# Performance work log

Hardware: AMD Instinct MI355X
Metric: run time of the kernel (lower is better)

Reference implementation:

```python
import jax, jax.numpy as jnp
import numpy as np

B_, C_, NH_, WS_, HID_ = 8, 512, 16, 7, 2048
HH, WW = 56, 56


def _rel_pos_index(ws):
    coords = np.stack(np.meshgrid(np.arange(ws), np.arange(ws), indexing='ij'))  # (2,ws,ws)
    cf = coords.reshape(2, -1)
    rc = (cf[:, :, None] - cf[:, None, :]).transpose(1, 2, 0)  # (ws2,ws2,2)
    rc[..., 0] += ws - 1
    rc[..., 1] += ws - 1
    rc[..., 0] *= 2 * ws - 1
    return jnp.asarray(rc.sum(-1).reshape(-1))  # (ws2*ws2,)


def _ln(x, g, b, eps):
    mu = x.mean(-1, keepdims=True)
    var = ((x - mu) ** 2).mean(-1, keepdims=True)
    return (x - mu) * jax.lax.rsqrt(var + eps) * g + b


def setup_inputs() -> dict:
    key = jax.random.key(0)
    ks = jax.random.split(key, 8)
    s = lambda k, shape: (jax.random.normal(k, shape, jnp.float32) * 0.02)
    return {
        'x': jax.random.normal(ks[0], (B_, HH * WW, C_), jnp.float32),
        'H': HH, 'W': WW,
        'norm1_g': jnp.ones((C_,), jnp.float32), 'norm1_b': jnp.zeros((C_,), jnp.float32),
        'norm2_g': jnp.ones((C_,), jnp.float32), 'norm2_b': jnp.zeros((C_,), jnp.float32),
        'qkv_w': s(ks[1], (3 * C_, C_)), 'qkv_b': jnp.zeros((3 * C_,), jnp.float32),
        'rpb': s(ks[2], ((2 * WS_ - 1) ** 2, NH_)),
        'fc1_w': s(ks[3], (HID_, C_)), 'fc1_b': jnp.zeros((HID_,), jnp.float32),
        'dw_w': s(ks[4], (HID_, 1, 3, 3)), 'dw_b': jnp.zeros((HID_,), jnp.float32),
        'fc2_w': s(ks[5], (C_, HID_)), 'fc2_b': jnp.zeros((C_,), jnp.float32),
    }


def reference(x, H, W, norm1_g, norm1_b, norm2_g, norm2_b, qkv_w, qkv_b, rpb,
              fc1_w, fc1_b, dw_w, dw_b, fc2_w, fc2_b):
    B, N, C = x.shape
    ws, nh = WS_, NH_
    hd = C // nh
    scale = hd ** -0.5
    ws2 = ws * ws
    nHw, nWw = H // ws, W // ws

    # ---- norm1 + WaveAttention (windowed attention w/ relative position bias) ----
    h = _ln(x, norm1_g, norm1_b, 1e-5)
    qkv = h @ qkv_w.T + qkv_b                                   # [B,N,3C]
    # window partition: [B, nH, ws, nW, ws, 3, nh, hd] -> [3, B*nH*nW, nh, ws2, hd]
    qkv = qkv.reshape(B, nHw, ws, nWw, ws, 3, nh, hd)
    qkv = qkv.transpose(5, 0, 1, 3, 6, 2, 4, 7).reshape(3, B * nHw * nWw, nh, ws2, hd)
    q, k, v = qkv[0], qkv[1], qkv[2]

    attn = jnp.einsum('wnid,wnjd->wnij', q, k) * scale          # [Bw,nh,ws2,ws2]
    bias = rpb[_rel_pos_index(ws)].reshape(ws2, ws2, nh).transpose(2, 0, 1)
    attn = jax.nn.softmax(attn + bias[None], axis=-1)
    out = jnp.einsum('wnij,wnjd->wnid', attn, v)                # [Bw,nh,ws2,hd]
    # window reverse
    out = out.transpose(0, 2, 1, 3).reshape(B, nHw, nWw, ws, ws, C)
    out = out.transpose(0, 1, 3, 2, 4, 5).reshape(B, N, C)
    x = x + out

    # ---- norm2 + PVT2FFN (fc1 -> depthwise 3x3 conv -> GELU -> fc2) ----
    h2 = _ln(x, norm2_g, norm2_b, 1e-5)
    h2 = h2 @ fc1_w.T + fc1_b                                   # [B,N,HID]
    img = h2.reshape(B, H, W, HID_).transpose(0, 3, 1, 2)       # [B,HID,H,W]
    img = jax.lax.conv_general_dilated(img, dw_w, (1, 1), 'SAME',
                                       feature_group_count=HID_)
    img = img + dw_b[None, :, None, None]
    h2 = img.reshape(B, HID_, N).transpose(0, 2, 1)
    h2 = jax.nn.gelu(h2, approximate=False)
    h2 = h2 @ fc2_w.T + fc2_b
    return x + h2
```

## Files before the change

kernel.cpp:

```cpp
#include <hip/hip_runtime.h>
#include <hip/hip_bf16.h>

typedef unsigned short u16;
typedef unsigned int u32;
typedef __attribute__((ext_vector_type(8))) short bf16x8_t;
typedef __attribute__((ext_vector_type(4))) float f32x4_t;
typedef __attribute__((ext_vector_type(8))) u16 u16x8;
typedef __attribute__((ext_vector_type(4))) u32 u32x4;

constexpr int B_  = 8;
constexpr int C_  = 512;
constexpr int NH_ = 16;
constexpr int HID_= 2048;
constexpr int Hh  = 56, Ww = 56;
constexpr int N_  = Hh * Ww;
constexpr int M_  = B_ * N_;

__device__ __forceinline__ u16 f2bf(float f) {
    u32 u = __float_as_uint(f);
    u32 r = (u + 0x7fffu + ((u >> 16) & 1u)) >> 16;
    return (u16)r;
}
__device__ __forceinline__ float bf2f(u16 v) {
    return __uint_as_float(((u32)v) << 16);
}

__device__ __forceinline__ void bar_raw() {
    __asm__ __volatile__("s_barrier" ::: "memory");
}

typedef const void __attribute__((address_space(1))) gvoid_t;
typedef void __attribute__((address_space(3))) lvoid_t;
__device__ __forceinline__ void gload16(const u16* g, u16* l) {
    __builtin_amdgcn_global_load_lds((gvoid_t*)g, (lvoid_t*)l, 16, 0, 0);
}

__global__ void cvt_w(const float* __restrict__ qkvw, const float* __restrict__ fc1w,
                      const float* __restrict__ fc2w, u16* __restrict__ oq,
                      u16* __restrict__ o1, u16* __restrict__ o2) {
    int i = blockIdx.x * 256 + threadIdx.x;
    if (i < 3 * C_ * C_) oq[i] = f2bf(qkvw[i]);
    if (i < HID_ * C_) { o1[i] = f2bf(fc1w[i]); o2[i] = f2bf(fc2w[i]); }
}

__global__ __launch_bounds__(256) void ln_kernel(const float* __restrict__ x,
        const float* __restrict__ g, const float* __restrict__ b, u16* __restrict__ out) {
    int lane = threadIdx.x & 63, wv = threadIdx.x >> 6;
    size_t row = (size_t)blockIdx.x * 4 + wv;
    const float4* xr = (const float4*)(x + row * C_);
    float4 a = xr[lane * 2], c = xr[lane * 2 + 1];
    float s  = a.x + a.y + a.z + a.w + c.x + c.y + c.z + c.w;
    float ss = a.x*a.x + a.y*a.y + a.z*a.z + a.w*a.w + c.x*c.x + c.y*c.y + c.z*c.z + c.w*c.w;
    #pragma unroll
    for (int off = 1; off < 64; off <<= 1) {
        s  += __shfl_xor(s, off);
        ss += __shfl_xor(ss, off);
    }
    float mean = s * (1.0f / C_);
    float var  = ss * (1.0f / C_) - mean * mean;
    float rstd = rsqrtf(var + 1e-5f);
    const float4* g4 = (const float4*)g;
    const float4* b4 = (const float4*)b;
    float4 g0 = g4[lane*2], g1 = g4[lane*2+1], b0 = b4[lane*2], b1 = b4[lane*2+1];
    u16x8 o;
    o[0] = f2bf((a.x - mean) * rstd * g0.x + b0.x);
    o[1] = f2bf((a.y - mean) * rstd * g0.y + b0.y);
    o[2] = f2bf((a.z - mean) * rstd * g0.z + b0.z);
    o[3] = f2bf((a.w - mean) * rstd * g0.w + b0.w);
    o[4] = f2bf((c.x - mean) * rstd * g1.x + b1.x);
    o[5] = f2bf((c.y - mean) * rstd * g1.y + b1.y);
    o[6] = f2bf((c.z - mean) * rstd * g1.z + b1.z);
    o[7] = f2bf((c.w - mean) * rstd * g1.w + b1.w);
    *(u16x8*)&out[row * C_ + lane * 8] = o;
}

template<bool RES, bool OUT_BF16>
__global__ __launch_bounds__(512) void gemm256(
        const u16* __restrict__ A, const u16* __restrict__ B,
        const float* __restrict__ bias, const float* __restrict__ res,
        void* __restrict__ Cout, int M, int N, int K,
        int nbm, int nbn) {
    const int nwg = nbm * nbn;
    const int id = blockIdx.x;
    const int xcd = id & 7, ii = id >> 3;
    const int q = nwg >> 3, r = nwg & 7;
    const int gidx = (xcd < r ? xcd * (q + 1) : r * (q + 1) + (xcd - r) * q) + ii;
    const int bm = gidx / nbn;
    const int bn = gidx - bm * nbn;

    __shared__ __align__(16) u16 As[2 * 16384];
    __shared__ __align__(16) u16 Bs[2 * 16384];
    const int tid = threadIdx.x;
    const int lane = tid & 63;
    const int w = tid >> 6;
    const int wm = w >> 2, wn = w & 3;

    const int r0 = lane >> 2;
    const int gcb = ((lane & 3) ^ ((lane >> 3) & 3));
    const int fr = lane & 15;
    const int g4 = lane >> 4;
    const int swz = (g4 ^ ((fr >> 1) & 3)) * 8;
    const int bhf = wn >> 1;
    const int bg0 = (wn & 1) * 4;

    const u16* aBase = A + (size_t)(bm * 256) * K;
    const u16* bBase = B + (size_t)(bn * 256) * K;

    f32x4_t acc[2][2][4][2];
    f32x4_t zero = {0.f, 0.f, 0.f, 0.f};
    #pragma unroll
    for (int a0 = 0; a0 < 2; a0++)
        #pragma unroll
        for (int b0 = 0; b0 < 2; b0++)
            #pragma unroll
            for (int c0 = 0; c0 < 4; c0++)
                #pragma unroll
                for (int d0 = 0; d0 < 2; d0++) acc[a0][b0][c0][d0] = zero;

    auto stage = [&](const u16* gb, u16* lb, int u, int hf) {
        const u16* src = gb + (size_t)(hf * 128 + w * 16 + r0) * K
                            + (size_t)(u * 64 + gcb * 8);
        u16* dst = lb + (u & 1) * 16384 + hf * 8192 + w * 512;
        gload16(src, dst);
        gload16(src + 32, dst + 4096);
    };

#define RD_A(DST, BB, QM)                                                      \
    _Pragma("unroll")                                                          \
    for (int ks = 0; ks < 2; ks++)                                             \
        _Pragma("unroll")                                                      \
        for (int mf = 0; mf < 4; mf++)                                         \
            DST[ks][mf] = *(const bf16x8_t*)&As[(BB) + wm * 8192 + ks * 4096   \
                            + ((QM) * 4 + mf) * 512 + fr * 32 + swz];

#define RD_B(DST, BB, QN)                                                      \
    _Pragma("unroll")                                                          \
    for (int ks = 0; ks < 2; ks++)                                             \
        _Pragma("unroll")                                                      \
        for (int nf = 0; nf < 2; nf++)                                         \
            DST[ks][nf] = *(const bf16x8_t*)&Bs[(BB) + bhf * 8192 + ks * 4096  \
                            + (bg0 + (QN) * 2 + nf) * 512 + fr * 32 + swz];

#define MMAC(QM, QN, AR, BR)                                                   \
    __builtin_amdgcn_s_setprio(1);                                             \
    _Pragma("unroll")                                                          \
    for (int mf = 0; mf < 4; mf++)                                             \
        _Pragma("unroll")                                                      \
        for (int nf = 0; nf < 2; nf++)                                         \
            _Pragma("unroll")                                                  \
            for (int ks = 0; ks < 2; ks++)                                     \
                acc[QM][QN][mf][nf] = __builtin_amdgcn_mfma_f32_16x16x32_bf16( \
                    AR[ks][mf], BR[ks][nf], acc[QM][QN][mf][nf], 0, 0, 0);     \
    __builtin_amdgcn_s_setprio(0);

    const int NT = K >> 6;
    stage(aBase, As, 0, 0);
    stage(aBase, As, 0, 1);
    stage(bBase, Bs, 0, 0);
    stage(bBase, Bs, 0, 1);
    stage(bBase, Bs, 1, 0);
    stage(aBase, As, 1, 0);
    __asm__ __volatile__("s_waitcnt vmcnt(0)" ::: "memory");
    bar_raw();

    bf16x8_t afr[2][4], bq0[2][2], bq1[2][2];
    RD_A(afr, 0, 0);
    RD_B(bq0, 0, 0);

    for (int t = 0; t < NT; t++) {
        const int bb = (t & 1) * 16384;
        const int ob = bb ^ 16384;
        MMAC(0, 0, afr, bq0);
        RD_B(bq1, bb, 1);
        if (t + 1 < NT) stage(aBase, As, t + 1, 1);
        bar_raw();
        MMAC(0, 1, afr, bq1);
        RD_A(afr, bb, 1);
        if (t + 1 < NT) stage(bBase, Bs, t + 1, 1);
        bar_raw();
        MMAC(1, 1, afr, bq1);
        if (t + 2 < NT) stage(bBase, Bs, t + 2, 0);
        bar_raw();
        MMAC(1, 0, afr, bq0);
        if (t + 2 < NT) {
            stage(aBase, As, t + 2, 0);
            __asm__ __volatile__("s_waitcnt vmcnt(4)" ::: "memory");
        } else if (t + 1 < NT) {
            __asm__ __volatile__("s_waitcnt vmcnt(0)" ::: "memory");
        }
        bar_raw();
        if (t + 1 < NT) {
            RD_A(afr, ob, 0);
            RD_B(bq0, ob, 0);
        }
    }

#undef RD_A
#undef RD_B
#undef MMAC

    #pragma unroll
    for (int qm = 0; qm < 2; qm++)
        #pragma unroll
        for (int qn = 0; qn < 2; qn++)
            #pragma unroll
            for (int mf = 0; mf < 4; mf++)
                #pragma unroll
                for (int rr = 0; rr < 4; rr++) {
                    int row = bm * 256 + wm * 128 + qm * 64 + mf * 16 + (lane >> 4) * 4 + rr;
                    #pragma unroll
                    for (int nf = 0; nf < 2; nf++) {
                        int col = bn * 256 + wn * 64 + qn * 32 + nf * 16 + (lane & 15);
                        float v = acc[qm][qn][mf][nf][rr] + bias[col];
                        if constexpr (RES) v += res[(size_t)row * N + col];
                        if constexpr (OUT_BF16) ((u16*)Cout)[(size_t)row * N + col] = f2bf(v);
                        else ((float*)Cout)[(size_t)row * N + col] = v;
                    }
                }
}

constexpr int QS = 40;
constexpr int VS = 72;
constexpr int PS = 72;

__global__ __launch_bounds__(256) void attn_kernel(
        const u16* __restrict__ qkv, const float* __restrict__ rpb,
        u16* __restrict__ aout) {
    __shared__ __align__(16) u16 q_s[64 * QS];
    __shared__ __align__(16) u16 k_s[64 * QS];
    __shared__ __align__(16) u16 vT_s[32 * VS];
    __shared__ __align__(16) u16 p_s[64 * PS];
    const int tid = threadIdx.x, lane = tid & 63, wv = tid >> 6;
    const int wh = blockIdx.x;
    const int head = wh & 15, w = wh >> 4;
    const int b = w >> 6, win = w & 63, bh = win >> 3, bw = win & 7;

    {
        int i = tid >> 2, dc = (tid & 3) * 8;
        if (i < 49) {
            int n = (bh * 7 + i / 7) * Ww + (bw * 7 + i % 7);
            const u16* base = qkv + ((size_t)(b * N_ + n)) * (3 * C_) + head * 32 + dc;
            *(u16x8*)&q_s[i * QS + dc] = *(const u16x8*)(base);
            *(u16x8*)&k_s[i * QS + dc] = *(const u16x8*)(base + C_);
        } else {
            u16x8 z = {0,0,0,0,0,0,0,0};
            *(u16x8*)&q_s[i * QS + dc] = z;
            *(u16x8*)&k_s[i * QS + dc] = z;
        }
    }
    for (int f = tid; f < 64 * 32; f += 256) {
        int i = f >> 5, d = f & 31;
        u16 val = 0;
        if (i < 49) {
            int n = (bh * 7 + i / 7) * Ww + (bw * 7 + i % 7);
            val = qkv[((size_t)(b * N_ + n)) * (3 * C_) + 2 * C_ + head * 32 + d];
        }
        vT_s[d * VS + i] = val;
    }
    __syncthreads();

    f32x4_t zero = {0.f, 0.f, 0.f, 0.f};
    f32x4_t s[4];
    bf16x8_t aq = *(const bf16x8_t*)&q_s[(wv * 16 + (lane & 15)) * QS + (lane >> 4) * 8];
    #pragma unroll
    for (int nt = 0; nt < 4; nt++) {
        bf16x8_t bk = *(const bf16x8_t*)&k_s[(nt * 16 + (lane & 15)) * QS + (lane >> 4) * 8];
        s[nt] = __builtin_amdgcn_mfma_f32_16x16x32_bf16(aq, bk, zero, 0, 0, 0);
    }

    const float scale = 0.17677669529663687f;
    #pragma unroll
    for (int r = 0; r < 4; r++) {
        int row = wv * 16 + (lane >> 4) * 4 + r;
        int qy = row / 7, qx = row - qy * 7;
        float pv[4];
        float m = -1e30f;
        #pragma unroll
        for (int nt = 0; nt < 4; nt++) {
            int col = nt * 16 + (lane & 15);
            float bias;
            if (row < 49 && col < 49) {
                int ky = col / 7, kx = col - ky * 7;
                bias = rpb[((qy - ky + 6) * 13 + (qx - kx + 6)) * NH_ + head];
            } else bias = -1e30f;
            float v = s[nt][r] * scale + bias;
            pv[nt] = v;
            m = fmaxf(m, v);
        }
        #pragma unroll
        for (int off = 1; off < 16; off <<= 1) m = fmaxf(m, __shfl_xor(m, off));
        float sum = 0.f;
        #pragma unroll
        for (int nt = 0; nt < 4; nt++) { pv[nt] = __expf(pv[nt] - m); sum += pv[nt]; }
        #pragma unroll
        for (int off = 1; off < 16; off <<= 1) sum += __shfl_xor(sum, off);
        float inv = 1.0f / sum;
        #pragma unroll
        for (int nt = 0; nt < 4; nt++)
            p_s[row * PS + nt * 16 + (lane & 15)] = f2bf(pv[nt] * inv);
    }
    __syncthreads();

    f32x4_t o[2] = {zero, zero};
    #pragma unroll
    for (int kt = 0; kt < 2; kt++) {
        bf16x8_t ap = *(const bf16x8_t*)&p_s[(wv * 16 + (lane & 15)) * PS + kt * 32 + (lane >> 4) * 8];
        #pragma unroll
        for (int nt = 0; nt < 2; nt++) {
            bf16x8_t bv = *(const bf16x8_t*)&vT_s[(nt * 16 + (lane & 15)) * VS + kt * 32 + (lane >> 4) * 8];
            o[nt] = __builtin_amdgcn_mfma_f32_16x16x32_bf16(ap, bv, o[nt], 0, 0, 0);
        }
    }
    u16* obase = aout + ((size_t)(w * 16 + head)) * 49 * 32;
    #pragma unroll
    for (int nt = 0; nt < 2; nt++) {
        #pragma unroll
        for (int r = 0; r < 4; r++) {
            int row = wv * 16 + (lane >> 4) * 4 + r;
            if (row < 49)
                obase[row * 32 + nt * 16 + (lane & 15)] = f2bf(o[nt][r]);
        }
    }
}

__global__ __launch_bounds__(256) void wrev_ln(const float* __restrict__ x,
        const u16* __restrict__ aout, const float* __restrict__ g,
        const float* __restrict__ bt, float* __restrict__ x2, u16* __restrict__ h) {
    int lane = threadIdx.x & 63, wvv = threadIdx.x >> 6;
    int m = blockIdx.x * 4 + wvv;
    int b = m / N_, n = m - b * N_;
    int iy = n / Ww, ix = n - iy * Ww;
    int w = b * 64 + (iy / 7) * 8 + (ix / 7);
    int pos = (iy % 7) * 7 + (ix % 7);
    int head = lane >> 2, d0 = (lane & 3) * 8;
    u16x8 ao = *(const u16x8*)&aout[(((size_t)w * 16 + head) * 49 + pos) * 32 + d0];
    const float4* xr = (const float4*)(x + (size_t)m * C_ + lane * 8);
    float4 a = xr[0], c = xr[1];
    float v[8];
    v[0] = a.x + bf2f(ao[0]); v[1] = a.y + bf2f(ao[1]);
    v[2] = a.z + bf2f(ao[2]); v[3] = a.w + bf2f(ao[3]);
    v[4] = c.x + bf2f(ao[4]); v[5] = c.y + bf2f(ao[5]);
    v[6] = c.z + bf2f(ao[6]); v[7] = c.w + bf2f(ao[7]);
    float s = 0.f, ss = 0.f;
    #pragma unroll
    for (int jj = 0; jj < 8; jj++) { s += v[jj]; ss += v[jj] * v[jj]; }
    #pragma unroll
    for (int off = 1; off < 64; off <<= 1) {
        s  += __shfl_xor(s, off);
        ss += __shfl_xor(ss, off);
    }
    float mean = s * (1.0f / C_);
    float var  = ss * (1.0f / C_) - mean * mean;
    float rstd = rsqrtf(var + 1e-5f);
    float4 o0 = {v[0], v[1], v[2], v[3]}, o1 = {v[4], v[5], v[6], v[7]};
    float4* x2r = (float4*)(x2 + (size_t)m * C_ + lane * 8);
    x2r[0] = o0; x2r[1] = o1;
    const float4* g4 = (const float4*)(g + lane * 8);
    const float4* b4 = (const float4*)(bt + lane * 8);
    float4 g0 = g4[0], g1 = g4[1], bb0 = b4[0], bb1 = b4[1];
    u16x8 o;
    o[0] = f2bf((v[0] - mean) * rstd * g0.x + bb0.x);
    o[1] = f2bf((v[1] - mean) * rstd * g0.y + bb0.y);
    o[2] = f2bf((v[2] - mean) * rstd * g0.z + bb0.z);
    o[3] = f2bf((v[3] - mean) * rstd * g0.w + bb0.w);
    o[4] = f2bf((v[4] - mean) * rstd * g1.x + bb1.x);
    o[5] = f2bf((v[5] - mean) * rstd * g1.y + bb1.y);
    o[6] = f2bf((v[6] - mean) * rstd * g1.z + bb1.z);
    o[7] = f2bf((v[7] - mean) * rstd * g1.w + bb1.w);
    *(u16x8*)&h[(size_t)m * C_ + lane * 8] = o;
}

__global__ __launch_bounds__(256) void dwconv_gelu(const u16* __restrict__ in,
        const float* __restrict__ w, const float* __restrict__ bias, u16* __restrict__ out) {
    const int t = threadIdx.x;
    const int blk = blockIdx.x;
    const int xq = blk & 3;
    const int byp = blk >> 2;
    const int yp = byp % 28;
    const int b = byp / 28;
    const int y0 = yp * 2;
    const int c0 = t * 8;

    float wr[9][8];
    #pragma unroll
    for (int k = 0; k < 9; k++)
        #pragma unroll
        for (int j = 0; j < 8; j++) wr[k][j] = w[(c0 + j) * 9 + k];
    float bs[8];
    #pragma unroll
    for (int j = 0; j < 8; j++) bs[j] = bias[c0 + j];

    u16x8 zerov = {0,0,0,0,0,0,0,0};
    auto ldcol = [&](int xx, u16x8* col) {
        #pragma unroll
        for (int dy = 0; dy < 4; dy++) {
            int yy = y0 + dy - 1;
            bool ok = (yy >= 0 && yy < Hh && xx >= 0 && xx < Ww);
            col[dy] = ok ? *(const u16x8*)&in[(((size_t)b * Hh + yy) * Ww + xx) * HID_ + c0] : zerov;
        }
    };

    int xs = xq * 14;
    u16x8 wA[4], wB[4], wC[4];
    ldcol(xs - 1, wA);
    ldcol(xs, wB);
    for (int x = xs; x < xs + 14; x++) {
        ldcol(x + 1, wC);
        float acc0[8], acc1[8];
        #pragma unroll
        for (int j = 0; j < 8; j++) { acc0[j] = bs[j]; acc1[j] = bs[j]; }
        #pragma unroll
        for (int dy = 0; dy < 3; dy++)
            #pragma unroll
            for (int j = 0; j < 8; j++) {
                acc0[j] += bf2f(wA[dy][j]) * wr[dy * 3 + 0][j];
                acc0[j] += bf2f(wB[dy][j]) * wr[dy * 3 + 1][j];
                acc0[j] += bf2f(wC[dy][j]) * wr[dy * 3 + 2][j];
                acc1[j] += bf2f(wA[dy + 1][j]) * wr[dy * 3 + 0][j];
                acc1[j] += bf2f(wB[dy + 1][j]) * wr[dy * 3 + 1][j];
                acc1[j] += bf2f(wC[dy + 1][j]) * wr[dy * 3 + 2][j];
            }
        u16x8 o0, o1;
        #pragma unroll
        for (int j = 0; j < 8; j++) {
            float v0 = acc0[j];
            o0[j] = f2bf(0.5f * v0 * (1.0f + erff(v0 * 0.70710678118654752f)));
            float v1 = acc1[j];
            o1[j] = f2bf(0.5f * v1 * (1.0f + erff(v1 * 0.70710678118654752f)));
        }
        *(u16x8*)&out[(((size_t)b * Hh + y0) * Ww + x) * HID_ + c0] = o0;
        *(u16x8*)&out[(((size_t)b * Hh + y0 + 1) * Ww + x) * HID_ + c0] = o1;
        #pragma unroll
        for (int dy = 0; dy < 4; dy++) { wA[dy] = wB[dy]; wB[dy] = wC[dy]; }
    }
}

extern "C" void kernel_launch(void* const* d_in, const int* in_sizes, int n_in,
                              void* d_out, int out_size, void* d_ws, size_t ws_size,
                              hipStream_t stream) {
    const float* x    = (const float*)d_in[0];
    const float* n1g  = (const float*)d_in[3];
    const float* n1b  = (const float*)d_in[4];
    const float* n2g  = (const float*)d_in[5];
    const float* n2b  = (const float*)d_in[6];
    const float* qkvw = (const float*)d_in[7];
    const float* qkvb = (const float*)d_in[8];
    const float* rpb  = (const float*)d_in[9];
    const float* fc1w = (const float*)d_in[10];
    const float* fc1b = (const float*)d_in[11];
    const float* dww  = (const float*)d_in[12];
    const float* dwb  = (const float*)d_in[13];
    const float* fc2w = (const float*)d_in[14];
    const float* fc2b = (const float*)d_in[15];

    char* ws = (char*)d_ws;
    float* x2  = (float*)(ws);
    u16*   h   = (u16*)(ws + 51380224);
    u16*   qkvo= (u16*)(ws + 77070336);
    u16*   aout= (u16*)(ws + 154140672);
    u16*   f1o = (u16*)(ws + 154140672);
    u16*   cvo = (u16*)(ws + 51380224);
    u16*   wq  = (u16*)(ws + 256901120);
    u16*   w1  = (u16*)(ws + 256901120 + 1572864);
    u16*   w2  = (u16*)(ws + 256901120 + 1572864 + 2097152);

    cvt_w<<<dim3(4096), dim3(256), 0, stream>>>(qkvw, fc1w, fc2w, wq, w1, w2);
    ln_kernel<<<dim3(M_ / 4), dim3(256), 0, stream>>>(x, n1g, n1b, h);
    gemm256<false, true><<<dim3(588), dim3(512), 0, stream>>>(
        h, wq, qkvb, nullptr, (void*)qkvo, M_, 1536, 512, 98, 6);
    attn_kernel<<<dim3(B_ * 64 * NH_), dim3(256), 0, stream>>>(qkvo, rpb, aout);
    wrev_ln<<<dim3(M_ / 4), dim3(256), 0, stream>>>(x, aout, n2g, n2b, x2, h);
    gemm256<false, true><<<dim3(784), dim3(512), 0, stream>>>(
        h, w1, fc1b, nullptr, (void*)f1o, M_, 2048, 512, 98, 8);
    dwconv_gelu<<<dim3(B_ * 28 * 4), dim3(256), 0, stream>>>(f1o, dww, dwb, cvo);
    gemm256<true, false><<<dim3(196), dim3(512), 0, stream>>>(
        cvo, w2, fc2b, x2, d_out, M_, 512, 2048, 98, 2);
}
```

Baseline: 510.1 us.

## Restructure GEMM main loop into triple-buffered K=32 stages with one barrier

Replaces the double-buffered K=64 LDS pipeline, which had four barriers per iteration, with a triple-buffered K=32 ring that uses one barrier per iteration and prefetches two stages ahead. Fragment loads now happen at the start of each iteration and the global loads are interleaved between MFMA groups. The aim is to cut barrier stalls and shrink LDS use, which could raise occupancy. In exchange each barrier covers half as much MFMA work, so loop overhead per FLOP goes up.

```diff
diff --git a/kernel.cpp b/kernel.cpp
--- a/kernel.cpp
+++ b/kernel.cpp
@@ -88,8 +88,8 @@
     const int bm = gidx / nbn;
     const int bn = gidx - bm * nbn;
 
-    __shared__ __align__(16) u16 As[2 * 16384];
-    __shared__ __align__(16) u16 Bs[2 * 16384];
+    __shared__ __align__(16) u16 As[3 * 8192];
+    __shared__ __align__(16) u16 Bs[3 * 8192];
     const int tid = threadIdx.x;
     const int lane = tid & 63;
     const int w = tid >> 6;
@@ -103,8 +103,9 @@
     const int bhf = wn >> 1;
     const int bg0 = (wn & 1) * 4;
 
-    const u16* aBase = A + (size_t)(bm * 256) * K;
-    const u16* bBase = B + (size_t)(bn * 256) * K;
+    const u16* aSrc = A + (size_t)(bm * 256 + w * 16 + r0) * K + gcb * 8;
+    const u16* bSrc = B + (size_t)(bn * 256 + w * 16 + r0) * K + gcb * 8;
+    const size_t hstep = (size_t)128 * K;
 
     f32x4_t acc[2][2][4][2];
     f32x4_t zero = {0.f, 0.f, 0.f, 0.f};
@@ -117,29 +118,24 @@
                 #pragma unroll
                 for (int d0 = 0; d0 < 2; d0++) acc[a0][b0][c0][d0] = zero;
 
-    auto stage = [&](const u16* gb, u16* lb, int u, int hf) {
-        const u16* src = gb + (size_t)(hf * 128 + w * 16 + r0) * K
-                            + (size_t)(u * 64 + gcb * 8);
-        u16* dst = lb + (u & 1) * 16384 + hf * 8192 + w * 512;
-        gload16(src, dst);
-        gload16(src + 32, dst + 4096);
+    auto stageA = [&](int u, int hf, int cb) {
+        gload16(aSrc + (size_t)hf * hstep + u * 32, &As[cb + hf * 4096 + w * 512]);
     };
-
-#define RD_A(DST, BB, QM)                                                      \
+    auto stageB = [&](int u, int hf, int cb) {
+        gload16(bSrc + (size_t)hf * hstep + u * 32, &Bs[cb + hf * 4096 + w * 512]);
+    };
+
+#define RD_A(DST, CB, QM)                                                      \
     _Pragma("unroll")                                                          \
-    for (int ks = 0; ks < 2; ks++)                                             \
-        _Pragma("unroll")                                                      \
-        for (int mf = 0; mf < 4; mf++)                                         \
-            DST[ks][mf] = *(const bf16x8_t*)&As[(BB) + wm * 8192 + ks * 4096   \
-                            + ((QM) * 4 + mf) * 512 + fr * 32 + swz];
-
-#define RD_B(DST, BB, QN)                                                      \
+    for (int mf = 0; mf < 4; mf++)                                             \
+        DST[mf] = *(const bf16x8_t*)&As[(CB) + wm * 4096                       \
+                        + ((QM) * 64 + mf * 16 + fr) * 32 + swz];
+
+#define RD_B(DST, CB, QN)                                                      \
     _Pragma("unroll")                                                          \
-    for (int ks = 0; ks < 2; ks++)                                             \
-        _Pragma("unroll")                                                      \
-        for (int nf = 0; nf < 2; nf++)                                         \
-            DST[ks][nf] = *(const bf16x8_t*)&Bs[(BB) + bhf * 8192 + ks * 4096  \
-                            + (bg0 + (QN) * 2 + nf) * 512 + fr * 32 + swz];
+    for (int nf = 0; nf < 2; nf++)                                             \
+        DST[nf] = *(const bf16x8_t*)&Bs[(CB) + bhf * 4096                      \
+                        + ((bg0 + (QN) * 2 + nf) * 16 + fr) * 32 + swz];
 
 #define MMAC(QM, QN, AR, BR)                                                   \
     __builtin_amdgcn_s_setprio(1);                                             \
@@ -147,52 +143,43 @@
     for (int mf = 0; mf < 4; mf++)                                             \
         _Pragma("unroll")                                                      \
         for (int nf = 0; nf < 2; nf++)                                         \
-            _Pragma("unroll")                                                  \
-            for (int ks = 0; ks < 2; ks++)                                     \
-                acc[QM][QN][mf][nf] = __builtin_amdgcn_mfma_f32_16x16x32_bf16( \
-                    AR[ks][mf], BR[ks][nf], acc[QM][QN][mf][nf], 0, 0, 0);     \
+            acc[QM][QN][mf][nf] = __builtin_amdgcn_mfma_f32_16x16x32_bf16(     \
+                AR[mf], BR[nf], acc[QM][QN][mf][nf], 0, 0, 0);                 \
     __builtin_amdgcn_s_setprio(0);
 
-    const int NT = K >> 6;
-    stage(aBase, As, 0, 0);
-    stage(aBase, As, 0, 1);
-    stage(bBase, Bs, 0, 0);
-    stage(bBase, Bs, 0, 1);
-    stage(bBase, Bs, 1, 0);
-    stage(aBase, As, 1, 0);
-    __asm__ __volatile__("s_waitcnt vmcnt(0)" ::: "memory");
+    const int NT = K >> 5;
+    stageA(0, 0, 0); stageA(0, 1, 0); stageB(0, 0, 0); stageB(0, 1, 0);
+    stageA(1, 0, 8192); stageA(1, 1, 8192); stageB(1, 0, 8192); stageB(1, 1, 8192);
+    __asm__ __volatile__("s_waitcnt vmcnt(4)" ::: "memory");
     bar_raw();
 
-    bf16x8_t afr[2][4], bq0[2][2], bq1[2][2];
-    RD_A(afr, 0, 0);
-    RD_B(bq0, 0, 0);
+    int cr = 0;
+    int cs = 2 * 8192;
+    bf16x8_t af0[4], af1[4], bq0[2], bq1[2];
 
     for (int t = 0; t < NT; t++) {
-        const int bb = (t & 1) * 16384;
-        const int ob = bb ^ 16384;
-        MMAC(0, 0, afr, bq0);
-        RD_B(bq1, bb, 1);
-        if (t + 1 < NT) stage(aBase, As, t + 1, 1);
+        RD_A(af0, cr, 0);
+        RD_B(bq0, cr, 0);
+        RD_B(bq1, cr, 1);
+        const bool st = (t + 2 < NT);
+        MMAC(0, 0, af0, bq0);
+        if (st) stageA(t + 2, 0, cs);
+        MMAC(0, 1, af0, bq1);
+        RD_A(af1, cr, 1);
+        if (st) stageA(t + 2, 1, cs);
+        MMAC(1, 1, af1, bq1);
+        if (st) stageB(t + 2, 0, cs);
+        MMAC(1, 0, af1, bq0);
+        if (st) stageB(t + 2, 1, cs);
+        if (t == NT - 1) break;
+        if (st) {
+            __asm__ __volatile__("s_waitcnt vmcnt(4)" ::: "memory");
+        } else {
+            __asm__ __volatile__("s_waitcnt vmcnt(0)" ::: "memory");
+        }
         bar_raw();
-        MMAC(0, 1, afr, bq1);
-        RD_A(afr, bb, 1);
-        if (t + 1 < NT) stage(bBase, Bs, t + 1, 1);
-        bar_raw();
-        MMAC(1, 1, afr, bq1);
-        if (t + 2 < NT) stage(bBase, Bs, t + 2, 0);
-        bar_raw();
-        MMAC(1, 0, afr, bq0);
-        if (t + 2 < NT) {
-            stage(aBase, As, t + 2, 0);
-            __asm__ __volatile__("s_waitcnt vmcnt(4)" ::: "memory");
-        } else if (t + 1 < NT) {
-            __asm__ __volatile__("s_waitcnt vmcnt(0)" ::: "memory");
-        }
-        bar_raw();
-        if (t + 1 < NT) {
-            RD_A(afr, ob, 0);
-            RD_B(bq0, ob, 0);
-        }
+        cr = (cr == 2 * 8192) ? 0 : cr + 8192;
+        cs = (cs == 2 * 8192) ? 0 : cs + 8192;
     }
 
 #undef RD_A
```

After: 535.4 us. +5.0%, slower.
